# Optimization experiments

Measured on AMD Instinct MI355X. Metric: run time of the kernel, lower is better.

The kernel has to match this reference:

```python
import jax, jax.numpy as jnp
import numpy as np

G = 512          # graphs per batch
NPG = 90         # nodes per graph (AAL-90 atlas)
N = G * NPG      # 46080 total nodes
DEG = 20
E = N * DEG      # 921600 edges
F_IN = 90
H = 64           # hidden_channels (args.hc)
K = 70           # sort-pool k


def setup_inputs() -> dict:
    key = jax.random.key(0)
    ks = jax.random.split(key, 14)
    x = jax.random.normal(ks[0], (N, F_IN), dtype=jnp.float32)
    # edges kept within each graph (realistic PyG batching)
    gid = jax.random.randint(ks[1], (E,), 0, G)
    src = gid * NPG + jax.random.randint(ks[2], (E,), 0, NPG)
    dst = gid * NPG + jax.random.randint(ks[3], (E,), 0, NPG)
    edge_index = jnp.stack([src, dst]).astype(jnp.int64)
    batch = (jnp.arange(N) // NPG).astype(jnp.int64)
    s_in = 1.0 / np.sqrt(F_IN)
    s_h = 1.0 / np.sqrt(H)
    s_p = 1.0 / np.sqrt(H * K)
    # SAGEConv: out = mean_aggr(x_j) @ W_l + x_i @ W_r + b
    W1l = jax.random.uniform(ks[4], (F_IN, H), jnp.float32, -s_in, s_in)
    W1r = jax.random.uniform(ks[5], (F_IN, H), jnp.float32, -s_in, s_in)
    b1 = jnp.zeros((H,), jnp.float32)
    W2l = jax.random.uniform(ks[6], (H, H), jnp.float32, -s_h, s_h)
    W2r = jax.random.uniform(ks[7], (H, H), jnp.float32, -s_h, s_h)
    b2 = jnp.zeros((H,), jnp.float32)
    Wl1 = jax.random.uniform(ks[8], (H * K, H), jnp.float32, -s_p, s_p)
    bl1 = jax.random.uniform(ks[9], (H,), jnp.float32, -s_p, s_p)
    Wl2 = jax.random.uniform(ks[10], (H, 1), jnp.float32, -s_h, s_h)
    bl2 = jax.random.uniform(ks[11], (1,), jnp.float32, -s_h, s_h)
    return {"x": x, "edge_index": edge_index, "batch": batch,
            "W1l": W1l, "W1r": W1r, "b1": b1,
            "W2l": W2l, "W2r": W2r, "b2": b2,
            "Wl1": Wl1, "bl1": bl1, "Wl2": Wl2, "bl2": bl2}


def sage_conv(x, src, dst, Wl, Wr, b):
    # gather source features, scatter-mean to destinations
    msg = x[src]                                              # [E, F]
    s = jax.ops.segment_sum(msg, dst, num_segments=N)         # [N, F]
    cnt = jax.ops.segment_sum(jnp.ones((src.shape[0], 1), x.dtype),
                              dst, num_segments=N)            # [N, 1]
    mean = s / jnp.maximum(cnt, 1.0)
    return mean @ Wl + x @ Wr + b


def global_sort_pool(x, k):
    # nodes per graph are contiguous and fixed (NPG >= k, no padding needed)
    xr = x.reshape(G, NPG, H)
    order = jnp.argsort(-xr[:, :, -1], axis=1)[:, :k]          # sort by last channel, desc
    top = jnp.take_along_axis(xr, order[:, :, None], axis=1)   # [G, k, H]
    return top.reshape(G, k * H)


def reference(x, edge_index, batch, W1l, W1r, b1, W2l, W2r, b2, Wl1, bl1, Wl2, bl2):
    src, dst = edge_index[0], edge_index[1]
    h = sage_conv(x, src, dst, W1l, W1r, b1)       # conv1
    x_train = h
    h = jax.nn.relu(h)
    h = sage_conv(h, src, dst, W2l, W2r, b2)       # conv2
    p = global_sort_pool(h, K)                     # [G, K*H]
    # dropout is identity at eval time
    p = p @ Wl1 + bl1
    p = p @ Wl2 + bl2
    out = jnp.squeeze(jax.nn.sigmoid(p))           # [G]
    return out, x_train
```

## Files before the change

### kernel.cpp

```cpp
#include <hip/hip_runtime.h>

typedef unsigned short u16;
typedef unsigned int u32;
typedef unsigned char u8;
typedef unsigned long long u64;

#define GG   512
#define NPG  90
#define NTOT (GG*NPG)
#define NED  921600
#define FIN  90
#define HC   64
#define KP   70
#define AW   23
#define AWG  (NPG*AW)

#define SAD  91
#define SP   68
#define SR   67

#define WF_W1L 0
#define WF_W1R 5760
#define WF_W2L 11520
#define WF_W2R 15616
#define WF_B1  19712
#define WF_B2  19776
#define WF_FOLD 19840
#define WF_ZC  24320
#define WF_FLAG 24321

__device__ __forceinline__ float bf2f(u16 u) {
    union { u32 i; float f; } v; v.i = ((u32)u) << 16; return v.f;
}
__device__ __forceinline__ float bflo(u32 u) {
    union { u32 i; float f; } v; v.i = u << 16; return v.f;
}
__device__ __forceinline__ float bfhi(u32 u) {
    union { u32 i; float f; } v; v.i = u & 0xFFFF0000u; return v.f;
}
__device__ __forceinline__ u16 f2bf(float f) {
    union { float f; u32 i; } v; v.f = f;
    u32 r = (v.i + 0x7FFFu + ((v.i >> 16) & 1u)) >> 16;
    return (u16)r;
}
__device__ __forceinline__ float ldadp(const void* p, long long i, int isf32) {
    return isf32 ? ((const float*)p)[i] : bf2f(((const u16*)p)[i]);
}

__global__ __launch_bounds__(256) void k_pre(
    const u32* __restrict__ xw, const int* __restrict__ ei,
    const void* W1l, const void* W1r, const void* b1,
    const void* W2l, const void* W2r, const void* b2,
    const void* Wl1, const void* bl1, const void* Wl2, const void* bl2,
    u32* __restrict__ A32, float* __restrict__ wf)
{
    __shared__ int sf;
    const int t = threadIdx.x;
    const int b = blockIdx.x;

    if (b < 900) {
        int lane = t & 63;
        u32 v = (lane < 16) ? (u32)ei[lane] : 0u;
        u64 bb = __ballot((lane & 1) && (v != 0));
        bool wide = (bb == 0ull);
        int e0 = b * 1024 + t * 4;
        int s[4], d[4];
        if (wide) {
            uint4 s01 = *(const uint4*)(ei + 2 * e0);
            uint4 s23 = *(const uint4*)(ei + 2 * e0 + 4);
            uint4 d01 = *(const uint4*)(ei + 2 * (NED + e0));
            uint4 d23 = *(const uint4*)(ei + 2 * (NED + e0) + 4);
            s[0] = (int)s01.x; s[1] = (int)s01.z; s[2] = (int)s23.x; s[3] = (int)s23.z;
            d[0] = (int)d01.x; d[1] = (int)d01.z; d[2] = (int)d23.x; d[3] = (int)d23.z;
        } else {
            uint4 ss = *(const uint4*)(ei + e0);
            uint4 dd = *(const uint4*)(ei + NED + e0);
            s[0] = (int)ss.x; s[1] = (int)ss.y; s[2] = (int)ss.z; s[3] = (int)ss.w;
            d[0] = (int)dd.x; d[1] = (int)dd.y; d[2] = (int)dd.z; d[3] = (int)dd.w;
        }
        #pragma unroll
        for (int k = 0; k < 4; ++k) {
            int dk = d[k];
            if ((unsigned)dk >= NTOT) continue;
            int g = (unsigned)dk / NPG;
            int dl = dk - g * NPG;
            int ls = s[k] - g * NPG;
            if ((unsigned)ls >= NPG) continue;
            atomicAdd(&A32[(size_t)g * AWG + dl * AW + (ls >> 2)],
                      1u << (8 * (ls & 3)));
        }
        return;
    }

    if (t < 64) {
        u32 e = (xw[t] >> 7) & 0xFF;
        u64 bb = __ballot(e >= 136);
        if (t == 0) sf = (bb != 0ull) ? 1 : 0;
    }
    __syncthreads();
    const int f32 = sf;

    if (b < 978) {
        int i = (b - 900) * 256 + t;
        if      (i < 5760)  wf[i] = ldadp(W1l, i, f32);
        else if (i < 11520) wf[i] = ldadp(W1r, i - 5760, f32);
        else if (i < 15616) wf[i] = ldadp(W2l, i - 11520, f32);
        else if (i < 19712) wf[i] = ldadp(W2r, i - 15616, f32);
        else if (i < 19776) wf[i] = ldadp(b1, i - 19712, f32);
        else if (i < 19840) wf[i] = ldadp(b2, i - 19776, f32);
        if (b == 900 && t == 0) wf[WF_FLAG] = f32 ? 1.0f : 0.0f;
    } else {
        int m = (b - 978) * 256 + t;
        if (m < 4480) {
            float s = 0.f;
            for (int j = 0; j < HC; ++j)
                s += ldadp(Wl1, (long long)m * HC + j, f32) * ldadp(Wl2, j, f32);
            wf[WF_FOLD + m] = s;
        } else if (m == 4480) {
            float s = ldadp(bl2, 0, f32);
            for (int j = 0; j < HC; ++j)
                s += ldadp(bl1, j, f32) * ldadp(Wl2, j, f32);
            wf[WF_ZC] = s;
        }
    }
}

__global__ __launch_bounds__(512, 4) void k_fused(
    const void* __restrict__ x, const u32* __restrict__ A32,
    const float* __restrict__ wf, void* __restrict__ dout)
{
    __shared__ __align__(16) char smem[58144];
    float* As    = (float*)smem;
    float* R1    = (float*)(smem + 32768);
    float* s_key = (float*)(smem + 57248);
    float* s_red = (float*)(smem + 57968);
    u16*   s_ord = (u16*)(smem + 58000);

    const int g = blockIdx.x;
    const int t = threadIdx.x;
    const bool isf32 = (wf[WF_FLAG] > 0.5f);

    const int l = t & 63;
    const int w = __builtin_amdgcn_readfirstlane(t >> 6);
    const int jb = w * 8;
    const int row0 = l;
    const bool has2 = (l < NPG - 64);
    const int row1 = has2 ? l + 64 : l;

    u32 abuf[5];
    {
        const u32* Ag = A32 + (size_t)g * AWG;
        #pragma unroll
        for (int j = 0; j < 5; ++j) {
            int p = t + j * 512;
            abuf[j] = (p < AWG) ? Ag[p] : 0u;
        }
    }

    if (isf32) {
        const float* xg = (const float*)x + (size_t)g * 8100;
        for (int p = t; p < 8100; p += 512) {
            int r = p / NPG, c = p - r * NPG;
            As[r * SAD + c] = xg[p];
        }
    } else {
        const u32* xg = (const u32*)((const u16*)x + (size_t)g * 8100);
        for (int p = t; p < 4050; p += 512) {
            int r = p / 45, c = (p - r * 45) * 2;
            u32 v = xg[p];
            As[r * SAD + c]     = bflo(v);
            As[r * SAD + c + 1] = bfhi(v);
        }
    }
    __syncthreads();

    float accP[2][8], accQ[2][8];
    {
        const float* bb = wf + WF_B1 + jb;
        #pragma unroll
        for (int j = 0; j < 8; ++j) {
            float bv = bb[j];
            accP[0][j] = 0.f; accP[1][j] = 0.f;
            accQ[0][j] = bv;  accQ[1][j] = bv;
        }
    }
    {
        const float* WL = wf + WF_W1L + jb;
        const float* WR = wf + WF_W1R + jb;
        #pragma unroll 3
        for (int k = 0; k < FIN; ++k) {
            float wl[8], wr[8];
            #pragma unroll
            for (int j = 0; j < 8; ++j) { wl[j] = WL[k * HC + j]; wr[j] = WR[k * HC + j]; }
            float x0 = As[row0 * SAD + k];
            float x1 = As[row1 * SAD + k];
            #pragma unroll
            for (int j = 0; j < 8; ++j) {
                accP[0][j] += x0 * wl[j]; accQ[0][j] += x0 * wr[j];
                accP[1][j] += x1 * wl[j]; accQ[1][j] += x1 * wr[j];
            }
        }
    }
    __syncthreads();

    *(float4*)(R1 + row0 * SP + jb)     = make_float4(accP[0][0], accP[0][1], accP[0][2], accP[0][3]);
    *(float4*)(R1 + row0 * SP + jb + 4) = make_float4(accP[0][4], accP[0][5], accP[0][6], accP[0][7]);
    if (has2) {
        *(float4*)(R1 + row1 * SP + jb)     = make_float4(accP[1][0], accP[1][1], accP[1][2], accP[1][3]);
        *(float4*)(R1 + row1 * SP + jb + 4) = make_float4(accP[1][4], accP[1][5], accP[1][6], accP[1][7]);
    }
    #pragma unroll
    for (int j = 0; j < 5; ++j) {
        int p = t + j * 512;
        if (p < AWG) {
            int r = p / AW, wc = p - r * AW;
            int c = wc * 4;
            u32 v = abuf[j];
            float* dst = As + r * SAD + c;
            dst[0] = (float)(v & 255u);
            dst[1] = (float)((v >> 8) & 255u);
            dst[2] = (float)((v >> 16) & 255u);
            if (c + 3 < SAD) dst[3] = (float)(v >> 24);
        }
    }
    __syncthreads();

    float r1v[2][8];
    float rc0, rc1;
    {
        float acc[2][8];
        float asum0 = 0.f, asum1 = 0.f;
        #pragma unroll
        for (int i = 0; i < 2; ++i)
            #pragma unroll
            for (int j = 0; j < 8; ++j) acc[i][j] = 0.f;
        for (int k = 0; k < NPG; ++k) {
            float4 p0 = *(const float4*)(R1 + k * SP + jb);
            float4 p1 = *(const float4*)(R1 + k * SP + jb + 4);
            float pv[8] = {p0.x,p0.y,p0.z,p0.w,p1.x,p1.y,p1.z,p1.w};
            float a0 = As[row0 * SAD + k];
            float a1 = As[row1 * SAD + k];
            asum0 += a0; asum1 += a1;
            #pragma unroll
            for (int j = 0; j < 8; ++j) {
                acc[0][j] += a0 * pv[j];
                acc[1][j] += a1 * pv[j];
            }
        }
        rc0 = 1.0f / fmaxf(asum0, 1.0f);
        rc1 = 1.0f / fmaxf(asum1, 1.0f);
        #pragma unroll
        for (int i = 0; i < 2; ++i) {
            if (i == 0 || has2) {
                int n = i ? row1 : row0;
                float rc = i ? rc1 : rc0;
                float h[8];
                #pragma unroll
                for (int j = 0; j < 8; ++j) h[j] = fmaf(rc, acc[i][j], accQ[i][j]);
                size_t base = 512 + (size_t)(g * NPG + n) * HC + jb;
                if (isf32) {
                    *(float4*)((float*)dout + base)     = make_float4(h[0],h[1],h[2],h[3]);
                    *(float4*)((float*)dout + base + 4) = make_float4(h[4],h[5],h[6],h[7]);
                } else {
                    uint4 pk;
                    pk.x = (u32)f2bf(h[0]) | ((u32)f2bf(h[1]) << 16);
                    pk.y = (u32)f2bf(h[2]) | ((u32)f2bf(h[3]) << 16);
                    pk.z = (u32)f2bf(h[4]) | ((u32)f2bf(h[5]) << 16);
                    pk.w = (u32)f2bf(h[6]) | ((u32)f2bf(h[7]) << 16);
                    *(uint4*)((u16*)dout + base) = pk;
                }
                #pragma unroll
                for (int j = 0; j < 8; ++j) r1v[i][j] = fmaxf(h[j], 0.f);
            }
        }
    }
    __syncthreads();
    #pragma unroll
    for (int j = 0; j < 8; ++j) R1[row0 * SR + jb + j] = r1v[0][j];
    if (has2) {
        #pragma unroll
        for (int j = 0; j < 8; ++j) R1[row1 * SR + jb + j] = r1v[1][j];
    }
    __syncthreads();

    {
        const float* bb = wf + WF_B2 + jb;
        #pragma unroll
        for (int j = 0; j < 8; ++j) {
            float bv = bb[j];
            accP[0][j] = 0.f; accP[1][j] = 0.f;
            accQ[0][j] = bv;  accQ[1][j] = bv;
        }
    }
    {
        const float* WL = wf + WF_W2L + jb;
        const float* WR = wf + WF_W2R + jb;
        #pragma unroll 4
        for (int k = 0; k < HC; ++k) {
            float wl[8], wr[8];
            #pragma unroll
            for (int j = 0; j < 8; ++j) { wl[j] = WL[k * HC + j]; wr[j] = WR[k * HC + j]; }
            float v0 = R1[row0 * SR + k];
            float v1 = R1[row1 * SR + k];
            #pragma unroll
            for (int j = 0; j < 8; ++j) {
                accP[0][j] += v0 * wl[j]; accQ[0][j] += v0 * wr[j];
                accP[1][j] += v1 * wl[j]; accQ[1][j] += v1 * wr[j];
            }
        }
    }
    __syncthreads();
    *(float4*)(R1 + row0 * SP + jb)     = make_float4(accP[0][0], accP[0][1], accP[0][2], accP[0][3]);
    *(float4*)(R1 + row0 * SP + jb + 4) = make_float4(accP[0][4], accP[0][5], accP[0][6], accP[0][7]);
    if (has2) {
        *(float4*)(R1 + row1 * SP + jb)     = make_float4(accP[1][0], accP[1][1], accP[1][2], accP[1][3]);
        *(float4*)(R1 + row1 * SP + jb + 4) = make_float4(accP[1][4], accP[1][5], accP[1][6], accP[1][7]);
    }
    __syncthreads();

    float h2v[2][8];
    {
        float acc[2][8];
        #pragma unroll
        for (int i = 0; i < 2; ++i)
            #pragma unroll
            for (int j = 0; j < 8; ++j) acc[i][j] = 0.f;
        for (int k = 0; k < NPG; ++k) {
            float4 p0 = *(const float4*)(R1 + k * SP + jb);
            float4 p1 = *(const float4*)(R1 + k * SP + jb + 4);
            float pv[8] = {p0.x,p0.y,p0.z,p0.w,p1.x,p1.y,p1.z,p1.w};
            float a0 = As[row0 * SAD + k];
            float a1 = As[row1 * SAD + k];
            #pragma unroll
            for (int j = 0; j < 8; ++j) {
                acc[0][j] += a0 * pv[j];
                acc[1][j] += a1 * pv[j];
            }
        }
        #pragma unroll
        for (int i = 0; i < 2; ++i) {
            if (i == 0 || has2) {
                int n = i ? row1 : row0;
                float rc = i ? rc1 : rc0;
                #pragma unroll
                for (int j = 0; j < 8; ++j)
                    h2v[i][j] = fmaf(rc, acc[i][j], accQ[i][j]);
                if (w == 7) s_key[n] = h2v[i][7];
            }
        }
    }
    __syncthreads();
    #pragma unroll
    for (int j = 0; j < 8; ++j) R1[row0 * SR + jb + j] = h2v[0][j];
    if (has2) {
        #pragma unroll
        for (int j = 0; j < 8; ++j) R1[row1 * SR + jb + j] = h2v[1][j];
    }
    if (t < NPG) {
        float my = s_key[t];
        int r = 0;
        for (int m2 = 0; m2 < NPG; ++m2) {
            float km = s_key[m2];
            r += (km > my) || (km == my && m2 < t);
        }
        if (r < KP) s_ord[r] = (u16)t;
    }
    __syncthreads();

    float zp = 0.f;
    for (int p = t; p < KP * HC; p += 512) {
        int i = p >> 6, c = p & 63;
        int nn = s_ord[i];
        zp += R1[nn * SR + c] * wf[WF_FOLD + p];
    }
    #pragma unroll
    for (int off = 32; off > 0; off >>= 1) zp += __shfl_down(zp, off);
    if ((t & 63) == 0) s_red[t >> 6] = zp;
    __syncthreads();
    if (t == 0) {
        float z = wf[WF_ZC];
        #pragma unroll
        for (int i = 0; i < 8; ++i) z += s_red[i];
        float sg = 1.0f / (1.0f + expf(-z));
        if (isf32) ((float*)dout)[g] = sg;
        else       ((u16*)dout)[g]   = f2bf(sg);
    }
}

extern "C" void kernel_launch(void* const* d_in, const int* in_sizes, int n_in,
                              void* d_out, int out_size, void* d_ws, size_t ws_size,
                              hipStream_t stream) {
    const void* x   = d_in[0];
    const int*  ei  = (const int*)d_in[1];
    const void* W1l = d_in[3];
    const void* W1r = d_in[4];
    const void* b1  = d_in[5];
    const void* W2l = d_in[6];
    const void* W2r = d_in[7];
    const void* b2  = d_in[8];
    const void* Wl1 = d_in[9];
    const void* bl1 = d_in[10];
    const void* Wl2 = d_in[11];
    const void* bl2 = d_in[12];

    char* ws    = (char*)d_ws;
    u32*  A32   = (u32*)ws;
    float* wf   = (float*)(ws + 4239360);

    hipMemsetAsync(A32, 0, 4239360, stream);
    k_pre<<<996, 256, 0, stream>>>((const u32*)x, ei, W1l, W1r, b1, W2l, W2r, b2,
                                   Wl1, bl1, Wl2, bl2, A32, wf);
    k_fused<<<GG, 512, 0, stream>>>(x, A32, wf, d_out);
}
```

Baseline: 185.5 us.

## Remap fused SAGE kernel to column-per-lane, 12-row-per-wave register tiling

Reassigns thread work so each lane owns one output channel and each wave owns a block of 12 nodes, replacing the previous 8-channel-by-2-row tiling. Stages W1 interleaved in LDS, reads inputs as float4 along k, and precomputes adjacency row-sum reciprocals up front from global memory. This is meant to cut LDS traffic per FMA and improve broadcast reuse. In exchange, LDS use grows to about 81 KB, which may reduce blocks per CU, and wave 7 overlaps wave 6's rows (78..89), so some rows are computed redundantly.

```diff
diff --git a/kernel.cpp b/kernel.cpp
--- a/kernel.cpp
+++ b/kernel.cpp
@@ -15,9 +15,7 @@
 #define AW   23
 #define AWG  (NPG*AW)
 
-#define SAD  91
-#define SP   68
-#define SR   67
+#define SAD  92
 
 #define WF_W1L 0
 #define WF_W1R 5760
@@ -28,6 +26,14 @@
 #define WF_FOLD 19840
 #define WF_ZC  24320
 #define WF_FLAG 24321
+
+#define LDS_REGA 0
+#define LDS_REGB 33120
+#define LDS_RCS  80224
+#define LDS_KEY  80592
+#define LDS_RED  80960
+#define LDS_ORD  80992
+#define LDS_TOT  81136
 
 __device__ __forceinline__ float bf2f(u16 u) {
     union { u32 i; float f; } v; v.i = ((u32)u) << 16; return v.f;
@@ -129,249 +135,238 @@
     const void* __restrict__ x, const u32* __restrict__ A32,
     const float* __restrict__ wf, void* __restrict__ dout)
 {
-    __shared__ __align__(16) char smem[58144];
-    float* As    = (float*)smem;
-    float* R1    = (float*)(smem + 32768);
-    float* s_key = (float*)(smem + 57248);
-    float* s_red = (float*)(smem + 57968);
-    u16*   s_ord = (u16*)(smem + 58000);
+    __shared__ __align__(16) char smem[LDS_TOT];
+    float* regA  = (float*)(smem + LDS_REGA);
+    float* regB  = (float*)(smem + LDS_REGB);
+    float* s_rcs = (float*)(smem + LDS_RCS);
+    float* s_key = (float*)(smem + LDS_KEY);
+    float* s_red = (float*)(smem + LDS_RED);
+    u16*   s_ord = (u16*)(smem + LDS_ORD);
 
     const int g = blockIdx.x;
     const int t = threadIdx.x;
     const bool isf32 = (wf[WF_FLAG] > 0.5f);
-
-    const int l = t & 63;
+    const int c = t & 63;
     const int w = __builtin_amdgcn_readfirstlane(t >> 6);
-    const int jb = w * 8;
-    const int row0 = l;
-    const bool has2 = (l < NPG - 64);
-    const int row1 = has2 ? l + 64 : l;
+    const int r0 = (w < 7) ? w * 12 : 78;
 
     u32 abuf[5];
-    {
-        const u32* Ag = A32 + (size_t)g * AWG;
-        #pragma unroll
-        for (int j = 0; j < 5; ++j) {
-            int p = t + j * 512;
-            abuf[j] = (p < AWG) ? Ag[p] : 0u;
-        }
+    const u32* Ag = A32 + (size_t)g * AWG;
+    #pragma unroll
+    for (int j = 0; j < 5; ++j) {
+        int p = t + j * 512;
+        abuf[j] = (p < AWG) ? Ag[p] : 0u;
+    }
+
+    if (t < NPG) {
+        const u32* Ar = Ag + t * AW;
+        u32 s = 0;
+        #pragma unroll
+        for (int i = 0; i < AW; ++i) {
+            u32 v = Ar[i];
+            s += (v & 255u) + ((v >> 8) & 255u) + ((v >> 16) & 255u) + (v >> 24);
+        }
+        s_rcs[t] = 1.0f / fmaxf((float)s, 1.0f);
     }
 
     if (isf32) {
         const float* xg = (const float*)x + (size_t)g * 8100;
         for (int p = t; p < 8100; p += 512) {
-            int r = p / NPG, c = p - r * NPG;
-            As[r * SAD + c] = xg[p];
+            int r = p / NPG, cc = p - r * NPG;
+            regA[r * SAD + cc] = xg[p];
         }
     } else {
         const u32* xg = (const u32*)((const u16*)x + (size_t)g * 8100);
         for (int p = t; p < 4050; p += 512) {
-            int r = p / 45, c = (p - r * 45) * 2;
+            int r = p / 45, cc = (p - r * 45) * 2;
             u32 v = xg[p];
-            As[r * SAD + c]     = bflo(v);
-            As[r * SAD + c + 1] = bfhi(v);
-        }
-    }
-    __syncthreads();
-
-    float accP[2][8], accQ[2][8];
-    {
-        const float* bb = wf + WF_B1 + jb;
-        #pragma unroll
-        for (int j = 0; j < 8; ++j) {
-            float bv = bb[j];
-            accP[0][j] = 0.f; accP[1][j] = 0.f;
-            accQ[0][j] = bv;  accQ[1][j] = bv;
-        }
-    }
-    {
-        const float* WL = wf + WF_W1L + jb;
-        const float* WR = wf + WF_W1R + jb;
-        #pragma unroll 3
-        for (int k = 0; k < FIN; ++k) {
-            float wl[8], wr[8];
-            #pragma unroll
-            for (int j = 0; j < 8; ++j) { wl[j] = WL[k * HC + j]; wr[j] = WR[k * HC + j]; }
-            float x0 = As[row0 * SAD + k];
-            float x1 = As[row1 * SAD + k];
-            #pragma unroll
-            for (int j = 0; j < 8; ++j) {
-                accP[0][j] += x0 * wl[j]; accQ[0][j] += x0 * wr[j];
-                accP[1][j] += x1 * wl[j]; accQ[1][j] += x1 * wr[j];
-            }
-        }
-    }
-    __syncthreads();
-
-    *(float4*)(R1 + row0 * SP + jb)     = make_float4(accP[0][0], accP[0][1], accP[0][2], accP[0][3]);
-    *(float4*)(R1 + row0 * SP + jb + 4) = make_float4(accP[0][4], accP[0][5], accP[0][6], accP[0][7]);
-    if (has2) {
-        *(float4*)(R1 + row1 * SP + jb)     = make_float4(accP[1][0], accP[1][1], accP[1][2], accP[1][3]);
-        *(float4*)(R1 + row1 * SP + jb + 4) = make_float4(accP[1][4], accP[1][5], accP[1][6], accP[1][7]);
+            regA[r * SAD + cc]     = bflo(v);
+            regA[r * SAD + cc + 1] = bfhi(v);
+        }
+    }
+    if (t < 180) regA[(t >> 1) * SAD + 90 + (t & 1)] = 0.f;
+
+    for (int idx = t; idx < 92 * 64; idx += 512) {
+        int k = idx >> 6, cc = idx & 63;
+        float wl = 0.f, wr = 0.f;
+        if (k < FIN) { wl = wf[WF_W1L + k * HC + cc]; wr = wf[WF_W1R + k * HC + cc]; }
+        *(float2*)(regB + k * 128 + 2 * cc) = make_float2(wl, wr);
+    }
+    __syncthreads();
+
+    float accP[12], accQ[12];
+    {
+        float bv = wf[WF_B1 + c];
+        #pragma unroll
+        for (int r = 0; r < 12; ++r) { accP[r] = 0.f; accQ[r] = bv; }
+    }
+    {
+        const float* Wp = regB + 2 * c;
+        const float* Xp = regA + r0 * SAD;
+        for (int k0 = 0; k0 < 23; ++k0) {
+            float2 w0 = *(const float2*)(Wp + k0 * 512);
+            float2 w1 = *(const float2*)(Wp + k0 * 512 + 128);
+            float2 w2 = *(const float2*)(Wp + k0 * 512 + 256);
+            float2 w3 = *(const float2*)(Wp + k0 * 512 + 384);
+            #pragma unroll
+            for (int r = 0; r < 12; ++r) {
+                float4 xv = *(const float4*)(Xp + r * SAD + k0 * 4);
+                accP[r] = fmaf(xv.x, w0.x, accP[r]);
+                accQ[r] = fmaf(xv.x, w0.y, accQ[r]);
+                accP[r] = fmaf(xv.y, w1.x, accP[r]);
+                accQ[r] = fmaf(xv.y, w1.y, accQ[r]);
+                accP[r] = fmaf(xv.z, w2.x, accP[r]);
+                accQ[r] = fmaf(xv.z, w2.y, accQ[r]);
+                accP[r] = fmaf(xv.w, w3.x, accP[r]);
+                accQ[r] = fmaf(xv.w, w3.y, accQ[r]);
+            }
+        }
+    }
+    __syncthreads();
+
+    #pragma unroll
+    for (int r = 0; r < 12; ++r) regB[(r0 + r) * HC + c] = accP[r];
+    if (t < 128) {
+        regB[90 * HC + t]        = 0.f;
+        regB[5888 + 90 * HC + t] = 0.f;
     }
     #pragma unroll
     for (int j = 0; j < 5; ++j) {
         int p = t + j * 512;
         if (p < AWG) {
             int r = p / AW, wc = p - r * AW;
-            int c = wc * 4;
             u32 v = abuf[j];
-            float* dst = As + r * SAD + c;
-            dst[0] = (float)(v & 255u);
-            dst[1] = (float)((v >> 8) & 255u);
-            dst[2] = (float)((v >> 16) & 255u);
-            if (c + 3 < SAD) dst[3] = (float)(v >> 24);
-        }
-    }
-    __syncthreads();
-
-    float r1v[2][8];
-    float rc0, rc1;
-    {
-        float acc[2][8];
-        float asum0 = 0.f, asum1 = 0.f;
-        #pragma unroll
-        for (int i = 0; i < 2; ++i)
-            #pragma unroll
-            for (int j = 0; j < 8; ++j) acc[i][j] = 0.f;
-        for (int k = 0; k < NPG; ++k) {
-            float4 p0 = *(const float4*)(R1 + k * SP + jb);
-            float4 p1 = *(const float4*)(R1 + k * SP + jb + 4);
-            float pv[8] = {p0.x,p0.y,p0.z,p0.w,p1.x,p1.y,p1.z,p1.w};
-            float a0 = As[row0 * SAD + k];
-            float a1 = As[row1 * SAD + k];
-            asum0 += a0; asum1 += a1;
-            #pragma unroll
-            for (int j = 0; j < 8; ++j) {
-                acc[0][j] += a0 * pv[j];
-                acc[1][j] += a1 * pv[j];
-            }
-        }
-        rc0 = 1.0f / fmaxf(asum0, 1.0f);
-        rc1 = 1.0f / fmaxf(asum1, 1.0f);
-        #pragma unroll
-        for (int i = 0; i < 2; ++i) {
-            if (i == 0 || has2) {
-                int n = i ? row1 : row0;
-                float rc = i ? rc1 : rc0;
-                float h[8];
-                #pragma unroll
-                for (int j = 0; j < 8; ++j) h[j] = fmaf(rc, acc[i][j], accQ[i][j]);
-                size_t base = 512 + (size_t)(g * NPG + n) * HC + jb;
-                if (isf32) {
-                    *(float4*)((float*)dout + base)     = make_float4(h[0],h[1],h[2],h[3]);
-                    *(float4*)((float*)dout + base + 4) = make_float4(h[4],h[5],h[6],h[7]);
-                } else {
-                    uint4 pk;
-                    pk.x = (u32)f2bf(h[0]) | ((u32)f2bf(h[1]) << 16);
-                    pk.y = (u32)f2bf(h[2]) | ((u32)f2bf(h[3]) << 16);
-                    pk.z = (u32)f2bf(h[4]) | ((u32)f2bf(h[5]) << 16);
-                    pk.w = (u32)f2bf(h[6]) | ((u32)f2bf(h[7]) << 16);
-                    *(uint4*)((u16*)dout + base) = pk;
-                }
-                #pragma unroll
-                for (int j = 0; j < 8; ++j) r1v[i][j] = fmaxf(h[j], 0.f);
-            }
-        }
-    }
-    __syncthreads();
-    #pragma unroll
-    for (int j = 0; j < 8; ++j) R1[row0 * SR + jb + j] = r1v[0][j];
-    if (has2) {
-        #pragma unroll
-        for (int j = 0; j < 8; ++j) R1[row1 * SR + jb + j] = r1v[1][j];
-    }
-    __syncthreads();
-
-    {
-        const float* bb = wf + WF_B2 + jb;
-        #pragma unroll
-        for (int j = 0; j < 8; ++j) {
-            float bv = bb[j];
-            accP[0][j] = 0.f; accP[1][j] = 0.f;
-            accQ[0][j] = bv;  accQ[1][j] = bv;
-        }
-    }
-    {
-        const float* WL = wf + WF_W2L + jb;
-        const float* WR = wf + WF_W2R + jb;
-        #pragma unroll 4
-        for (int k = 0; k < HC; ++k) {
-            float wl[8], wr[8];
-            #pragma unroll
-            for (int j = 0; j < 8; ++j) { wl[j] = WL[k * HC + j]; wr[j] = WR[k * HC + j]; }
-            float v0 = R1[row0 * SR + k];
-            float v1 = R1[row1 * SR + k];
-            #pragma unroll
-            for (int j = 0; j < 8; ++j) {
-                accP[0][j] += v0 * wl[j]; accQ[0][j] += v0 * wr[j];
-                accP[1][j] += v1 * wl[j]; accQ[1][j] += v1 * wr[j];
-            }
-        }
-    }
-    __syncthreads();
-    *(float4*)(R1 + row0 * SP + jb)     = make_float4(accP[0][0], accP[0][1], accP[0][2], accP[0][3]);
-    *(float4*)(R1 + row0 * SP + jb + 4) = make_float4(accP[0][4], accP[0][5], accP[0][6], accP[0][7]);
-    if (has2) {
-        *(float4*)(R1 + row1 * SP + jb)     = make_float4(accP[1][0], accP[1][1], accP[1][2], accP[1][3]);
-        *(float4*)(R1 + row1 * SP + jb + 4) = make_float4(accP[1][4], accP[1][5], accP[1][6], accP[1][7]);
-    }
-    __syncthreads();
-
-    float h2v[2][8];
-    {
-        float acc[2][8];
-        #pragma unroll
-        for (int i = 0; i < 2; ++i)
-            #pragma unroll
-            for (int j = 0; j < 8; ++j) acc[i][j] = 0.f;
-        for (int k = 0; k < NPG; ++k) {
-            float4 p0 = *(const float4*)(R1 + k * SP + jb);
-            float4 p1 = *(const float4*)(R1 + k * SP + jb + 4);
-            float pv[8] = {p0.x,p0.y,p0.z,p0.w,p1.x,p1.y,p1.z,p1.w};
-            float a0 = As[row0 * SAD + k];
-            float a1 = As[row1 * SAD + k];
-            #pragma unroll
-            for (int j = 0; j < 8; ++j) {
-                acc[0][j] += a0 * pv[j];
-                acc[1][j] += a1 * pv[j];
-            }
-        }
-        #pragma unroll
-        for (int i = 0; i < 2; ++i) {
-            if (i == 0 || has2) {
-                int n = i ? row1 : row0;
-                float rc = i ? rc1 : rc0;
-                #pragma unroll
-                for (int j = 0; j < 8; ++j)
-                    h2v[i][j] = fmaf(rc, acc[i][j], accQ[i][j]);
-                if (w == 7) s_key[n] = h2v[i][7];
-            }
-        }
-    }
-    __syncthreads();
-    #pragma unroll
-    for (int j = 0; j < 8; ++j) R1[row0 * SR + jb + j] = h2v[0][j];
-    if (has2) {
-        #pragma unroll
-        for (int j = 0; j < 8; ++j) R1[row1 * SR + jb + j] = h2v[1][j];
-    }
+            *(float4*)(regA + r * SAD + wc * 4) = make_float4(
+                (float)(v & 255u), (float)((v >> 8) & 255u),
+                (float)((v >> 16) & 255u), (float)(v >> 24));
+        }
+    }
+    __syncthreads();
+
+    float h1[12];
+    {
+        float acc[12];
+        #pragma unroll
+        for (int r = 0; r < 12; ++r) acc[r] = 0.f;
+        const float* Ap = regA + r0 * SAD;
+        const float* Pp = regB + c;
+        for (int k0 = 0; k0 < 23; ++k0) {
+            float p0 = Pp[(4 * k0 + 0) * HC];
+            float p1 = Pp[(4 * k0 + 1) * HC];
+            float p2 = Pp[(4 * k0 + 2) * HC];
+            float p3 = Pp[(4 * k0 + 3) * HC];
+            #pragma unroll
+            for (int r = 0; r < 12; ++r) {
+                float4 av = *(const float4*)(Ap + r * SAD + k0 * 4);
+                acc[r] = fmaf(av.x, p0, acc[r]);
+                acc[r] = fmaf(av.y, p1, acc[r]);
+                acc[r] = fmaf(av.z, p2, acc[r]);
+                acc[r] = fmaf(av.w, p3, acc[r]);
+            }
+        }
+        if (isf32) {
+            #pragma unroll
+            for (int r = 0; r < 12; ++r) {
+                float h = fmaf(s_rcs[r0 + r], acc[r], accQ[r]);
+                ((float*)dout)[512 + (size_t)(g * NPG + r0 + r) * HC + c] = h;
+                h1[r] = fmaxf(h, 0.f);
+            }
+        } else {
+            #pragma unroll
+            for (int r = 0; r < 12; ++r) {
+                float h = fmaf(s_rcs[r0 + r], acc[r], accQ[r]);
+                ((u16*)dout)[512 + (size_t)(g * NPG + r0 + r) * HC + c] = f2bf(h);
+                h1[r] = fmaxf(h, 0.f);
+            }
+        }
+    }
+    __syncthreads();
+
+    #pragma unroll
+    for (int r = 0; r < 12; ++r) regB[(r0 + r) * HC + c] = h1[r];
+    float accQ2[12];
+    {
+        float bv = wf[WF_B2 + c];
+        #pragma unroll
+        for (int r = 0; r < 12; ++r) { accP[r] = 0.f; accQ2[r] = bv; }
+        const float* WL = wf + WF_W2L + c;
+        const float* WR = wf + WF_W2R + c;
+        const float* Rp = regB + r0 * HC;
+        for (int k0 = 0; k0 < 16; ++k0) {
+            float wl0 = WL[(4 * k0 + 0) * HC], wr0 = WR[(4 * k0 + 0) * HC];
+            float wl1 = WL[(4 * k0 + 1) * HC], wr1 = WR[(4 * k0 + 1) * HC];
+            float wl2 = WL[(4 * k0 + 2) * HC], wr2 = WR[(4 * k0 + 2) * HC];
+            float wl3 = WL[(4 * k0 + 3) * HC], wr3 = WR[(4 * k0 + 3) * HC];
+            #pragma unroll
+            for (int r = 0; r < 12; ++r) {
+                float4 rv = *(const float4*)(Rp + r * HC + k0 * 4);
+                accP[r]  = fmaf(rv.x, wl0, accP[r]);
+                accQ2[r] = fmaf(rv.x, wr0, accQ2[r]);
+                accP[r]  = fmaf(rv.y, wl1, accP[r]);
+                accQ2[r] = fmaf(rv.y, wr1, accQ2[r]);
+                accP[r]  = fmaf(rv.z, wl2, accP[r]);
+                accQ2[r] = fmaf(rv.z, wr2, accQ2[r]);
+                accP[r]  = fmaf(rv.w, wl3, accP[r]);
+                accQ2[r] = fmaf(rv.w, wr3, accQ2[r]);
+            }
+        }
+    }
+    {
+        float* P2 = regB + 5888;
+        #pragma unroll
+        for (int r = 0; r < 12; ++r) P2[(r0 + r) * HC + c] = accP[r];
+    }
+    __syncthreads();
+
+    float h2v[12];
+    {
+        float acc[12];
+        #pragma unroll
+        for (int r = 0; r < 12; ++r) acc[r] = 0.f;
+        const float* Ap = regA + r0 * SAD;
+        const float* Pp = regB + 5888 + c;
+        for (int k0 = 0; k0 < 23; ++k0) {
+            float p0 = Pp[(4 * k0 + 0) * HC];
+            float p1 = Pp[(4 * k0 + 1) * HC];
+            float p2 = Pp[(4 * k0 + 2) * HC];
+            float p3 = Pp[(4 * k0 + 3) * HC];
+            #pragma unroll
+            for (int r = 0; r < 12; ++r) {
+                float4 av = *(const float4*)(Ap + r * SAD + k0 * 4);
+                acc[r] = fmaf(av.x, p0, acc[r]);
+                acc[r] = fmaf(av.y, p1, acc[r]);
+                acc[r] = fmaf(av.z, p2, acc[r]);
+                acc[r] = fmaf(av.w, p3, acc[r]);
+            }
+        }
+        #pragma unroll
+        for (int r = 0; r < 12; ++r)
+            h2v[r] = fmaf(s_rcs[r0 + r], acc[r], accQ2[r]);
+        if (c == 63) {
+            #pragma unroll
+            for (int r = 0; r < 12; ++r) s_key[r0 + r] = h2v[r];
+        }
+    }
+    __syncthreads();
+
+    #pragma unroll
+    for (int r = 0; r < 12; ++r) regB[(r0 + r) * HC + c] = h2v[r];
     if (t < NPG) {
         float my = s_key[t];
-        int r = 0;
+        int rk = 0;
         for (int m2 = 0; m2 < NPG; ++m2) {
             float km = s_key[m2];
-            r += (km > my) || (km == my && m2 < t);
-        }
-        if (r < KP) s_ord[r] = (u16)t;
+            rk += (km > my) || (km == my && m2 < t);
+        }
+        if (rk < KP) s_ord[rk] = (u16)t;
     }
     __syncthreads();
 
     float zp = 0.f;
     for (int p = t; p < KP * HC; p += 512) {
-        int i = p >> 6, c = p & 63;
+        int i = p >> 6, cc = p & 63;
         int nn = s_ord[i];
-        zp += R1[nn * SR + c] * wf[WF_FOLD + p];
+        zp += regB[nn * HC + cc] * wf[WF_FOLD + p];
     }
     #pragma unroll
     for (int off = 32; off > 0; off >>= 1) zp += __shfl_down(zp, off);
```

Result: slower. 196.8 us (+6.1%).

## Keep adjacency packed in LDS and vectorize row reads with float4

Applied to the files above, without the earlier changes.

Adjacency bytes are no longer expanded to floats in shared memory. They stay as packed u32 words and are unpacked in registers, so each LDS read covers four neighbors. The feature and hidden row buffers are padded (SAD=92, reuse of stride SP) so the dense matmul loops can read four k-values per float4 LDS load instead of scalar loads. Shared memory grows by about 9 KB per block, and there is extra integer shift/convert work in the aggregation loops.

```diff
diff --git a/kernel.cpp b/kernel.cpp
--- a/kernel.cpp
+++ b/kernel.cpp
@@ -15,9 +15,9 @@
 #define AW   23
 #define AWG  (NPG*AW)
 
-#define SAD  91
+#define SAD  92
 #define SP   68
-#define SR   67
+#define APW  25
 
 #define WF_W1L 0
 #define WF_W1R 5760
@@ -129,12 +129,13 @@
     const void* __restrict__ x, const u32* __restrict__ A32,
     const float* __restrict__ wf, void* __restrict__ dout)
 {
-    __shared__ __align__(16) char smem[58144];
+    __shared__ __align__(16) char smem[67136];
     float* As    = (float*)smem;
-    float* R1    = (float*)(smem + 32768);
-    float* s_key = (float*)(smem + 57248);
-    float* s_red = (float*)(smem + 57968);
-    u16*   s_ord = (u16*)(smem + 58000);
+    float* R1    = (float*)(smem + 33120);
+    u32*   Apk   = (u32*)(smem + 57600);
+    float* s_key = (float*)(smem + 66600);
+    float* s_red = (float*)(smem + 66960);
+    u16*   s_ord = (u16*)(smem + 66992);
 
     const int g = blockIdx.x;
     const int t = threadIdx.x;
@@ -172,6 +173,15 @@
             As[r * SAD + c + 1] = bfhi(v);
         }
     }
+    if (t < 180) As[(t >> 1) * SAD + 90 + (t & 1)] = 0.f;
+    #pragma unroll
+    for (int j = 0; j < 5; ++j) {
+        int p = t + j * 512;
+        if (p < AWG) {
+            int r = p / AW, wc = p - r * AW;
+            Apk[r * APW + wc] = abuf[j];
+        }
+    }
     __syncthreads();
 
     float accP[2][8], accQ[2][8];
@@ -187,17 +197,24 @@
     {
         const float* WL = wf + WF_W1L + jb;
         const float* WR = wf + WF_W1R + jb;
-        #pragma unroll 3
-        for (int k = 0; k < FIN; ++k) {
-            float wl[8], wr[8];
-            #pragma unroll
-            for (int j = 0; j < 8; ++j) { wl[j] = WL[k * HC + j]; wr[j] = WR[k * HC + j]; }
-            float x0 = As[row0 * SAD + k];
-            float x1 = As[row1 * SAD + k];
-            #pragma unroll
-            for (int j = 0; j < 8; ++j) {
-                accP[0][j] += x0 * wl[j]; accQ[0][j] += x0 * wr[j];
-                accP[1][j] += x1 * wl[j]; accQ[1][j] += x1 * wr[j];
+        const float* X0 = As + row0 * SAD;
+        const float* X1 = As + row1 * SAD;
+        for (int k0 = 0; k0 < 23; ++k0) {
+            float4 q0 = *(const float4*)(X0 + 4 * k0);
+            float4 q1 = *(const float4*)(X1 + 4 * k0);
+            float xa0[4] = {q0.x, q0.y, q0.z, q0.w};
+            float xa1[4] = {q1.x, q1.y, q1.z, q1.w};
+            #pragma unroll
+            for (int jj = 0; jj < 4; ++jj) {
+                int k = 4 * k0 + jj;
+                float wl[8], wr[8];
+                #pragma unroll
+                for (int j = 0; j < 8; ++j) { wl[j] = WL[k * HC + j]; wr[j] = WR[k * HC + j]; }
+                #pragma unroll
+                for (int j = 0; j < 8; ++j) {
+                    accP[0][j] += xa0[jj] * wl[j]; accQ[0][j] += xa0[jj] * wr[j];
+                    accP[1][j] += xa1[jj] * wl[j]; accQ[1][j] += xa1[jj] * wr[j];
+                }
             }
         }
     }
@@ -209,20 +226,6 @@
         *(float4*)(R1 + row1 * SP + jb)     = make_float4(accP[1][0], accP[1][1], accP[1][2], accP[1][3]);
         *(float4*)(R1 + row1 * SP + jb + 4) = make_float4(accP[1][4], accP[1][5], accP[1][6], accP[1][7]);
     }
-    #pragma unroll
-    for (int j = 0; j < 5; ++j) {
-        int p = t + j * 512;
-        if (p < AWG) {
-            int r = p / AW, wc = p - r * AW;
-            int c = wc * 4;
-            u32 v = abuf[j];
-            float* dst = As + r * SAD + c;
-            dst[0] = (float)(v & 255u);
-            dst[1] = (float)((v >> 8) & 255u);
-            dst[2] = (float)((v >> 16) & 255u);
-            if (c + 3 < SAD) dst[3] = (float)(v >> 24);
-        }
-    }
     __syncthreads();
 
     float r1v[2][8];
@@ -234,17 +237,42 @@
         for (int i = 0; i < 2; ++i)
             #pragma unroll
             for (int j = 0; j < 8; ++j) acc[i][j] = 0.f;
-        for (int k = 0; k < NPG; ++k) {
-            float4 p0 = *(const float4*)(R1 + k * SP + jb);
-            float4 p1 = *(const float4*)(R1 + k * SP + jb + 4);
-            float pv[8] = {p0.x,p0.y,p0.z,p0.w,p1.x,p1.y,p1.z,p1.w};
-            float a0 = As[row0 * SAD + k];
-            float a1 = As[row1 * SAD + k];
-            asum0 += a0; asum1 += a1;
-            #pragma unroll
-            for (int j = 0; j < 8; ++j) {
-                acc[0][j] += a0 * pv[j];
-                acc[1][j] += a1 * pv[j];
+        const u32* A0 = Apk + row0 * APW;
+        const u32* A1 = Apk + row1 * APW;
+        for (int k0 = 0; k0 < 22; ++k0) {
+            u32 w0 = A0[k0], w1 = A1[k0];
+            #pragma unroll
+            for (int jj = 0; jj < 4; ++jj) {
+                int k = 4 * k0 + jj;
+                float4 p0 = *(const float4*)(R1 + k * SP + jb);
+                float4 p1 = *(const float4*)(R1 + k * SP + jb + 4);
+                float pv[8] = {p0.x,p0.y,p0.z,p0.w,p1.x,p1.y,p1.z,p1.w};
+                float a0 = (float)((w0 >> (8 * jj)) & 255u);
+                float a1 = (float)((w1 >> (8 * jj)) & 255u);
+                asum0 += a0; asum1 += a1;
+                #pragma unroll
+                for (int j = 0; j < 8; ++j) {
+                    acc[0][j] += a0 * pv[j];
+                    acc[1][j] += a1 * pv[j];
+                }
+            }
+        }
+        {
+            u32 w0 = A0[22], w1 = A1[22];
+            #pragma unroll
+            for (int jj = 0; jj < 2; ++jj) {
+                int k = 88 + jj;
+                float4 p0 = *(const float4*)(R1 + k * SP + jb);
+                float4 p1 = *(const float4*)(R1 + k * SP + jb + 4);
+                float pv[8] = {p0.x,p0.y,p0.z,p0.w,p1.x,p1.y,p1.z,p1.w};
+                float a0 = (float)((w0 >> (8 * jj)) & 255u);
+                float a1 = (float)((w1 >> (8 * jj)) & 255u);
+                asum0 += a0; asum1 += a1;
+                #pragma unroll
+                for (int j = 0; j < 8; ++j) {
+                    acc[0][j] += a0 * pv[j];
+                    acc[1][j] += a1 * pv[j];
+                }
             }
         }
         rc0 = 1.0f / fmaxf(asum0, 1.0f);
@@ -275,11 +303,11 @@
         }
     }
     __syncthreads();
-    #pragma unroll
-    for (int j = 0; j < 8; ++j) R1[row0 * SR + jb + j] = r1v[0][j];
+    *(float4*)(R1 + row0 * SP + jb)     = make_float4(r1v[0][0], r1v[0][1], r1v[0][2], r1v[0][3]);
+    *(float4*)(R1 + row0 * SP + jb + 4) = make_float4(r1v[0][4], r1v[0][5], r1v[0][6], r1v[0][7]);
     if (has2) {
-        #pragma unroll
-        for (int j = 0; j < 8; ++j) R1[row1 * SR + jb + j] = r1v[1][j];
+        *(float4*)(R1 + row1 * SP + jb)     = make_float4(r1v[1][0], r1v[1][1], r1v[1][2], r1v[1][3]);
+        *(float4*)(R1 + row1 * SP + jb + 4) = make_float4(r1v[1][4], r1v[1][5], r1v[1][6], r1v[1][7]);
     }
     __syncthreads();
 
@@ -295,17 +323,24 @@
     {
         const float* WL = wf + WF_W2L + jb;
         const float* WR = wf + WF_W2R + jb;
-        #pragma unroll 4
-        for (int k = 0; k < HC; ++k) {
-            float wl[8], wr[8];
-            #pragma unroll
-            for (int j = 0; j < 8; ++j) { wl[j] = WL[k * HC + j]; wr[j] = WR[k * HC + j]; }
-            float v0 = R1[row0 * SR + k];
-            float v1 = R1[row1 * SR + k];
-            #pragma unroll
-            for (int j = 0; j < 8; ++j) {
-                accP[0][j] += v0 * wl[j]; accQ[0][j] += v0 * wr[j];
-                accP[1][j] += v1 * wl[j]; accQ[1][j] += v1 * wr[j];
+        const float* V0 = R1 + row0 * SP;
+        const float* V1 = R1 + row1 * SP;
+        for (int k0 = 0; k0 < 16; ++k0) {
+            float4 q0 = *(const float4*)(V0 + 4 * k0);
+            float4 q1 = *(const float4*)(V1 + 4 * k0);
+            float va0[4] = {q0.x, q0.y, q0.z, q0.w};
+            float va1[4] = {q1.x, q1.y, q1.z, q1.w};
+            #pragma unroll
+            for (int jj = 0; jj < 4; ++jj) {
+                int k = 4 * k0 + jj;
+                float wl[8], wr[8];
+                #pragma unroll
+                for (int j = 0; j < 8; ++j) { wl[j] = WL[k * HC + j]; wr[j] = WR[k * HC + j]; }
+                #pragma unroll
+                for (int j = 0; j < 8; ++j) {
+                    accP[0][j] += va0[jj] * wl[j]; accQ[0][j] += va0[jj] * wr[j];
+                    accP[1][j] += va1[jj] * wl[j]; accQ[1][j] += va1[jj] * wr[j];
+                }
             }
         }
     }
@@ -325,16 +360,40 @@
         for (int i = 0; i < 2; ++i)
             #pragma unroll
             for (int j = 0; j < 8; ++j) acc[i][j] = 0.f;
-        for (int k = 0; k < NPG; ++k) {
-            float4 p0 = *(const float4*)(R1 + k * SP + jb);
-            float4 p1 = *(const float4*)(R1 + k * SP + jb + 4);
-            float pv[8] = {p0.x,p0.y,p0.z,p0.w,p1.x,p1.y,p1.z,p1.w};
-            float a0 = As[row0 * SAD + k];
-            float a1 = As[row1 * SAD + k];
-            #pragma unroll
-            for (int j = 0; j < 8; ++j) {
-                acc[0][j] += a0 * pv[j];
-                acc[1][j] += a1 * pv[j];
+        const u32* A0 = Apk + row0 * APW;
+        const u32* A1 = Apk + row1 * APW;
+        for (int k0 = 0; k0 < 22; ++k0) {
+            u32 w0 = A0[k0], w1 = A1[k0];
+            #pragma unroll
+            for (int jj = 0; jj < 4; ++jj) {
+                int k = 4 * k0 + jj;
+                float4 p0 = *(const float4*)(R1 + k * SP + jb);
+                float4 p1 = *(const float4*)(R1 + k * SP + jb + 4);
+                float pv[8] = {p0.x,p0.y,p0.z,p0.w,p1.x,p1.y,p1.z,p1.w};
+                float a0 = (float)((w0 >> (8 * jj)) & 255u);
+                float a1 = (float)((w1 >> (8 * jj)) & 255u);
+                #pragma unroll
+                for (int j = 0; j < 8; ++j) {
+                    acc[0][j] += a0 * pv[j];
+                    acc[1][j] += a1 * pv[j];
+                }
+            }
+        }
+        {
+            u32 w0 = A0[22], w1 = A1[22];
+            #pragma unroll
+            for (int jj = 0; jj < 2; ++jj) {
+                int k = 88 + jj;
+                float4 p0 = *(const float4*)(R1 + k * SP + jb);
+                float4 p1 = *(const float4*)(R1 + k * SP + jb + 4);
+                float pv[8] = {p0.x,p0.y,p0.z,p0.w,p1.x,p1.y,p1.z,p1.w};
+                float a0 = (float)((w0 >> (8 * jj)) & 255u);
+                float a1 = (float)((w1 >> (8 * jj)) & 255u);
+                #pragma unroll
+                for (int j = 0; j < 8; ++j) {
+                    acc[0][j] += a0 * pv[j];
+                    acc[1][j] += a1 * pv[j];
+                }
             }
         }
         #pragma unroll
@@ -350,11 +409,11 @@
         }
     }
     __syncthreads();
-    #pragma unroll
-    for (int j = 0; j < 8; ++j) R1[row0 * SR + jb + j] = h2v[0][j];
+    *(float4*)(R1 + row0 * SP + jb)     = make_float4(h2v[0][0], h2v[0][1], h2v[0][2], h2v[0][3]);
+    *(float4*)(R1 + row0 * SP + jb + 4) = make_float4(h2v[0][4], h2v[0][5], h2v[0][6], h2v[0][7]);
     if (has2) {
-        #pragma unroll
-        for (int j = 0; j < 8; ++j) R1[row1 * SR + jb + j] = h2v[1][j];
+        *(float4*)(R1 + row1 * SP + jb)     = make_float4(h2v[1][0], h2v[1][1], h2v[1][2], h2v[1][3]);
+        *(float4*)(R1 + row1 * SP + jb + 4) = make_float4(h2v[1][4], h2v[1][5], h2v[1][6], h2v[1][7]);
     }
     if (t < NPG) {
         float my = s_key[t];
@@ -371,7 +430,7 @@
     for (int p = t; p < KP * HC; p += 512) {
         int i = p >> 6, c = p & 63;
         int nn = s_ord[i];
-        zp += R1[nn * SR + c] * wf[WF_FOLD + p];
+        zp += R1[nn * SP + c] * wf[WF_FOLD + p];
     }
     #pragma unroll
     for (int off = 32; off > 0; off >>= 1) zp += __shfl_down(zp, off);
```

Measured after the change: 186.1 us. No clear change (+0.3%).
